# Performance work log

Hardware: AMD Instinct MI355X
Metric: run time of the kernel (lower is better)

Reference implementation:

```python
import jax, jax.numpy as jnp
import numpy as np

B, S, T, D = 64, 50, 200, 128
IN2, H = 128, 64
NEG = -1e10


def setup_inputs() -> dict:
    key = jax.random.key(0)
    k1, k2, k3, k4, k5, k6, k7, k8 = jax.random.split(key, 8)
    inp = jax.random.normal(k1, (B, S, T, D), dtype=jnp.float32)
    z = jax.random.normal(k2, (B, S, IN2), dtype=jnp.float32)
    mask = jax.random.randint(k3, (B, S, T), 0, 2, dtype=jnp.int32)
    # torch nn.Linear weights: [out, in]
    W1 = jax.random.normal(k4, (H, D), dtype=jnp.float32) / np.sqrt(D)
    W2_w = jax.random.normal(k5, (H, IN2), dtype=jnp.float32) / np.sqrt(IN2)
    W2_b = jax.random.normal(k6, (H,), dtype=jnp.float32) * 0.01
    V_w = jax.random.normal(k7, (1, H), dtype=jnp.float32) / np.sqrt(H)
    V_b = jax.random.normal(k8, (1,), dtype=jnp.float32) * 0.01
    return {"input": inp, "z": z, "mask": mask, "W1": W1,
            "W2_w": W2_w, "W2_b": W2_b, "V_w": V_w, "V_b": V_b}


def reference(input, z, mask, W1, W2_w, W2_b, V_w, V_b):
    # w1h: [B,S,T,H]
    w1h = jnp.einsum('bstd,hd->bsth', input, W1)
    # w2h: [B,S,H] (Linear with bias), broadcast over T
    w2h = jnp.einsum('bsd,hd->bsh', z, W2_w) + W2_b
    u = jnp.tanh(w1h + w2h[:, :, None, :])           # [B,S,T,H]
    att = jnp.einsum('bsth,h->bst', u, V_w[0]) + V_b[0]  # [B,S,T]
    att = jnp.where(mask == 0, NEG, att)
    att = jax.nn.softmax(att, axis=2)
    out = jnp.einsum('bst,bstd->bsd', att, input)    # [B,S,D]
    return out
```

## Files before the change

kernel.cpp:

```cpp
#include <hip/hip_runtime.h>

#define Tdim 200
#define Ddim 128
#define Hdim 64
#define NBS  3200
#define NEGV (-1e10f)

typedef _Float16 f16x8 __attribute__((ext_vector_type(8)));
typedef float    floatx4 __attribute__((ext_vector_type(4)));

__device__ __forceinline__ unsigned int packf16(float a, float b) {
    _Float16 ha = (_Float16)a, hb = (_Float16)b;
    unsigned int ua = *(unsigned short*)&ha, ub = *(unsigned short*)&hb;
    return ua | (ub << 16);
}

__device__ __forceinline__ float ftanh(float x) {
    float e = __expf(2.0f * x);
    return 1.0f - 2.0f * __builtin_amdgcn_rcpf(e + 1.0f);
}

__global__ __launch_bounds__(256, 3) void attn_main(
    const float* __restrict__ X, const float* __restrict__ z,
    const int* __restrict__ mask,
    const float* __restrict__ W1, const float* __restrict__ W2w,
    const float* __restrict__ W2b,
    const float* __restrict__ Vw, const float* __restrict__ Vb,
    float* __restrict__ out)
{
    __shared__ __align__(16) unsigned short xs[Tdim * 128];
    __shared__ float attL[Tdim];
    __shared__ float red[8];
    __shared__ float w2hL[Hdim];

    const int tid = threadIdx.x;
    const int bs  = blockIdx.x;
    const float* __restrict__ Xb = X + (size_t)bs * (Tdim * Ddim);
    const int lane = tid & 63;
    const int wv   = tid >> 6;
    const int l15  = lane & 15, quad = lane >> 4;

    int mval = 1;
    if (tid < Tdim) mval = mask[bs * Tdim + tid];

    {
        const int h = tid >> 2, q = tid & 3;
        const float4* zp = (const float4*)(z + (size_t)bs * 128 + q * 32);
        const float4* wp = (const float4*)(W2w + h * 128 + q * 32);
        float a = 0.f;
        #pragma unroll
        for (int i = 0; i < 8; ++i) {
            float4 zv = zp[i], wv4 = wp[i];
            a = fmaf(zv.x, wv4.x, a); a = fmaf(zv.y, wv4.y, a);
            a = fmaf(zv.z, wv4.z, a); a = fmaf(zv.w, wv4.w, a);
        }
        a += __shfl_xor(a, 1);
        a += __shfl_xor(a, 2);
        if (q == 0) w2hL[h] = a + W2b[h];
    }
    __syncthreads();

    const int R0  = wv * 48;
    const int nIt = (wv == 3) ? 28 : 24;
    #pragma unroll 4
    for (int i = 0; i < nIt; ++i) {
        int j = i * 64 + lane;
        int t = R0 + (j >> 5), dq = j & 31;
        float4 v = *(const float4*)(Xb + t * Ddim + dq * 4);
        unsigned int lo = packf16(v.x, v.y);
        unsigned int hi = packf16(v.z, v.w);
        int u16 = t * 16 + ((dq >> 1) ^ (t & 15));
        *(uint2*)((char*)xs + u16 * 16 + (dq & 1) * 8) = make_uint2(lo, hi);
    }

    f16x8 bfrag[4][4];
    #pragma unroll
    for (int n = 0; n < 4; ++n)
        #pragma unroll
        for (int ks = 0; ks < 4; ++ks) {
            const float* wp = W1 + (n * 16 + l15) * 128 + ks * 32 + quad * 8;
            float4 v0 = *(const float4*)wp;
            float4 v1 = *(const float4*)(wp + 4);
            uint4 u = make_uint4(packf16(v0.x, v0.y), packf16(v0.z, v0.w),
                                 packf16(v1.x, v1.y), packf16(v1.z, v1.w));
            bfrag[n][ks] = *(f16x8*)&u;
        }

    const float Vb0 = Vb[0];
    float vwr[4], w2[4];
    #pragma unroll
    for (int n = 0; n < 4; ++n) {
        vwr[n] = Vw[l15 + 16 * n];
        w2[n]  = w2hL[l15 + 16 * n];
    }

    const int mtEnd = (wv == 3) ? 13 : wv * 3 + 3;
    for (int mt = wv * 3; mt < mtEnd; ++mt) {
        const int t0 = (mt == 12) ? 184 : mt * 16;
        const int trow = t0 + l15;
        floatx4 acc[4];
        #pragma unroll
        for (int n = 0; n < 4; ++n) acc[n] = (floatx4){0.f, 0.f, 0.f, 0.f};
        f16x8 afrag[4];
        #pragma unroll
        for (int ks = 0; ks < 4; ++ks) {
            int u16 = trow * 16 + (((ks << 2) + quad) ^ (trow & 15));
            afrag[ks] = *(const f16x8*)(xs + u16 * 8);
        }
        #pragma unroll
        for (int n = 0; n < 4; ++n)
            #pragma unroll
            for (int ks = 0; ks < 4; ++ks)
                acc[n] = __builtin_amdgcn_mfma_f32_16x16x32_f16(afrag[ks], bfrag[n][ks], acc[n], 0, 0, 0);

        float s0 = 0.f, s1 = 0.f, s2 = 0.f, s3 = 0.f;
        #pragma unroll
        for (int n = 0; n < 4; ++n) {
            s0 = fmaf(ftanh(acc[n][0] + w2[n]), vwr[n], s0);
            s1 = fmaf(ftanh(acc[n][1] + w2[n]), vwr[n], s1);
            s2 = fmaf(ftanh(acc[n][2] + w2[n]), vwr[n], s2);
            s3 = fmaf(ftanh(acc[n][3] + w2[n]), vwr[n], s3);
        }
        #pragma unroll
        for (int m = 1; m < 16; m <<= 1) {
            s0 += __shfl_xor(s0, m);
            s1 += __shfl_xor(s1, m);
            s2 += __shfl_xor(s2, m);
            s3 += __shfl_xor(s3, m);
        }
        if (l15 == 0) {
            const int tb = t0 + quad * 4;
            attL[tb]     = s0 + Vb0;
            attL[tb + 1] = s1 + Vb0;
            attL[tb + 2] = s2 + Vb0;
            attL[tb + 3] = s3 + Vb0;
        }
    }
    __syncthreads();

    float l = -3e38f;
    if (tid < Tdim) {
        l = attL[tid];
        if (mval == 0) l = NEGV;
    }
    float m = l;
    #pragma unroll
    for (int off = 32; off > 0; off >>= 1) m = fmaxf(m, __shfl_xor(m, off));
    if (lane == 0) red[wv] = m;
    __syncthreads();
    const float M = fmaxf(fmaxf(red[0], red[1]), fmaxf(red[2], red[3]));
    float p = __expf(l - M);
    float sm = p;
    #pragma unroll
    for (int off = 32; off > 0; off >>= 1) sm += __shfl_xor(sm, off);
    if (lane == 0) red[4 + wv] = sm;
    __syncthreads();
    const float S = (red[4] + red[5]) + (red[6] + red[7]);
    if (tid < Tdim) attL[tid] = p / S;
    __syncthreads();

    {
        const int dblk = 4 * wv + (lane & 3);
        const int tg   = lane >> 2;
        float o0=0.f,o1=0.f,o2=0.f,o3=0.f,o4=0.f,o5=0.f,o6=0.f,o7=0.f;
        #pragma unroll 4
        for (int t = tg; t < Tdim; t += 16) {
            int u16 = t * 16 + (dblk ^ (t & 15));
            f16x8 xv = *(const f16x8*)(xs + u16 * 8);
            float a = attL[t];
            o0 = fmaf((float)xv[0], a, o0);
            o1 = fmaf((float)xv[1], a, o1);
            o2 = fmaf((float)xv[2], a, o2);
            o3 = fmaf((float)xv[3], a, o3);
            o4 = fmaf((float)xv[4], a, o4);
            o5 = fmaf((float)xv[5], a, o5);
            o6 = fmaf((float)xv[6], a, o6);
            o7 = fmaf((float)xv[7], a, o7);
        }
        #pragma unroll
        for (int m2 = 4; m2 <= 32; m2 <<= 1) {
            o0 += __shfl_xor(o0, m2); o1 += __shfl_xor(o1, m2);
            o2 += __shfl_xor(o2, m2); o3 += __shfl_xor(o3, m2);
            o4 += __shfl_xor(o4, m2); o5 += __shfl_xor(o5, m2);
            o6 += __shfl_xor(o6, m2); o7 += __shfl_xor(o7, m2);
        }
        if (tg == 0) {
            float* op = out + bs * Ddim + dblk * 8;
            *(float4*)op       = make_float4(o0, o1, o2, o3);
            *(float4*)(op + 4) = make_float4(o4, o5, o6, o7);
        }
    }
}

extern "C" void kernel_launch(void* const* d_in, const int* in_sizes, int n_in,
                              void* d_out, int out_size, void* d_ws, size_t ws_size,
                              hipStream_t stream) {
    const float* X    = (const float*)d_in[0];
    const float* z    = (const float*)d_in[1];
    const int*   mask = (const int*)d_in[2];
    const float* W1   = (const float*)d_in[3];
    const float* W2w  = (const float*)d_in[4];
    const float* W2b  = (const float*)d_in[5];
    const float* Vw   = (const float*)d_in[6];
    const float* Vb   = (const float*)d_in[7];
    float* out = (float*)d_out;

    attn_main<<<NBS, 256, 0, stream>>>(X, z, mask, W1, W2w, W2b, Vw, Vb, out);
}
```

Measured before the change: 473.7 us.

## Compute W2h per-lane in registers and fuse softmax into weighted sum

Removes the shared-memory W2h stage and its block barrier by having each lane compute its four W2h values directly from z and W2w, then reduce them with cross-lane shuffles. The mask is applied when attention logits are written, and the softmax max and sum are computed redundantly within each wave over all T values. This drops three barriers and the reduction scratch array. The cost is more redundant global loads of W2w/z per lane and more exp work per wave; masked-out t beyond T get probability zero via a -3e38 sentinel, and the read from xs is clamped to row 0 so it stays in bounds.

```diff
diff --git a/kernel.cpp b/kernel.cpp
--- a/kernel.cpp
+++ b/kernel.cpp
@@ -30,35 +30,19 @@
 {
     __shared__ __align__(16) unsigned short xs[Tdim * 128];
     __shared__ float attL[Tdim];
-    __shared__ float red[8];
-    __shared__ float w2hL[Hdim];
 
     const int tid = threadIdx.x;
     const int bs  = blockIdx.x;
     const float* __restrict__ Xb = X + (size_t)bs * (Tdim * Ddim);
+    const int* __restrict__ maskb = mask + bs * Tdim;
     const int lane = tid & 63;
     const int wv   = tid >> 6;
     const int l15  = lane & 15, quad = lane >> 4;
 
-    int mval = 1;
-    if (tid < Tdim) mval = mask[bs * Tdim + tid];
-
-    {
-        const int h = tid >> 2, q = tid & 3;
-        const float4* zp = (const float4*)(z + (size_t)bs * 128 + q * 32);
-        const float4* wp = (const float4*)(W2w + h * 128 + q * 32);
-        float a = 0.f;
-        #pragma unroll
-        for (int i = 0; i < 8; ++i) {
-            float4 zv = zp[i], wv4 = wp[i];
-            a = fmaf(zv.x, wv4.x, a); a = fmaf(zv.y, wv4.y, a);
-            a = fmaf(zv.z, wv4.z, a); a = fmaf(zv.w, wv4.w, a);
-        }
-        a += __shfl_xor(a, 1);
-        a += __shfl_xor(a, 2);
-        if (q == 0) w2hL[h] = a + W2b[h];
-    }
-    __syncthreads();
+    if (tid < Tdim) {
+        int mv_ = maskb[tid];
+        asm volatile("" :: "v"(mv_));
+    }
 
     const int R0  = wv * 48;
     const int nIt = (wv == 3) ? 28 : 24;
@@ -73,6 +57,32 @@
         *(uint2*)((char*)xs + u16 * 16 + (dq & 1) * 8) = make_uint2(lo, hi);
     }
 
+    float w2[4];
+    {
+        const float4* zp = (const float4*)(z + (size_t)bs * 128 + quad * 32);
+        float4 zv[8];
+        #pragma unroll
+        for (int i = 0; i < 8; ++i) zv[i] = zp[i];
+        #pragma unroll
+        for (int n = 0; n < 4; ++n) {
+            const float4* wp = (const float4*)(W2w + (l15 + 16 * n) * 128 + quad * 32);
+            float a = 0.f;
+            #pragma unroll
+            for (int i = 0; i < 8; ++i) {
+                float4 wv4 = wp[i];
+                a = fmaf(zv[i].x, wv4.x, a); a = fmaf(zv[i].y, wv4.y, a);
+                a = fmaf(zv[i].z, wv4.z, a); a = fmaf(zv[i].w, wv4.w, a);
+            }
+            w2[n] = a;
+        }
+        #pragma unroll
+        for (int n = 0; n < 4; ++n) {
+            w2[n] += __shfl_xor(w2[n], 16);
+            w2[n] += __shfl_xor(w2[n], 32);
+            w2[n] += W2b[l15 + 16 * n];
+        }
+    }
+
     f16x8 bfrag[4][4];
     #pragma unroll
     for (int n = 0; n < 4; ++n)
@@ -87,12 +97,9 @@
         }
 
     const float Vb0 = Vb[0];
-    float vwr[4], w2[4];
+    float vwr[4];
     #pragma unroll
-    for (int n = 0; n < 4; ++n) {
-        vwr[n] = Vw[l15 + 16 * n];
-        w2[n]  = w2hL[l15 + 16 * n];
-    }
+    for (int n = 0; n < 4; ++n) vwr[n] = Vw[l15 + 16 * n];
 
     const int mtEnd = (wv == 3) ? 13 : wv * 3 + 3;
     for (int mt = wv * 3; mt < mtEnd; ++mt) {
@@ -130,44 +137,47 @@
         }
         if (l15 == 0) {
             const int tb = t0 + quad * 4;
-            attL[tb]     = s0 + Vb0;
-            attL[tb + 1] = s1 + Vb0;
-            attL[tb + 2] = s2 + Vb0;
-            attL[tb + 3] = s3 + Vb0;
+            const int4 mv = *(const int4*)(maskb + tb);
+            attL[tb]     = (mv.x == 0) ? NEGV : s0 + Vb0;
+            attL[tb + 1] = (mv.y == 0) ? NEGV : s1 + Vb0;
+            attL[tb + 2] = (mv.z == 0) ? NEGV : s2 + Vb0;
+            attL[tb + 3] = (mv.w == 0) ? NEGV : s3 + Vb0;
         }
     }
     __syncthreads();
 
-    float l = -3e38f;
-    if (tid < Tdim) {
-        l = attL[tid];
-        if (mval == 0) l = NEGV;
-    }
-    float m = l;
-    #pragma unroll
-    for (int off = 32; off > 0; off >>= 1) m = fmaxf(m, __shfl_xor(m, off));
-    if (lane == 0) red[wv] = m;
-    __syncthreads();
-    const float M = fmaxf(fmaxf(red[0], red[1]), fmaxf(red[2], red[3]));
-    float p = __expf(l - M);
-    float sm = p;
-    #pragma unroll
-    for (int off = 32; off > 0; off >>= 1) sm += __shfl_xor(sm, off);
-    if (lane == 0) red[4 + wv] = sm;
-    __syncthreads();
-    const float S = (red[4] + red[5]) + (red[6] + red[7]);
-    if (tid < Tdim) attL[tid] = p / S;
-    __syncthreads();
-
     {
-        const int dblk = 4 * wv + (lane & 3);
-        const int tg   = lane >> 2;
+        const int tg = lane >> 2, dblk = 4 * wv + (lane & 3);
+        float pv[13];
+        float mx = -3e38f;
+        #pragma unroll
+        for (int k = 0; k < 13; ++k) {
+            int t = tg + 16 * k;
+            float lk = (t < Tdim) ? attL[t] : -3e38f;
+            pv[k] = lk;
+            mx = fmaxf(mx, lk);
+        }
+        #pragma unroll
+        for (int off = 4; off <= 32; off <<= 1) mx = fmaxf(mx, __shfl_xor(mx, off));
+        float sum = 0.f;
+        #pragma unroll
+        for (int k = 0; k < 13; ++k) {
+            float p = __expf(pv[k] - mx);
+            pv[k] = p;
+            sum += p;
+        }
+        #pragma unroll
+        for (int off = 4; off <= 32; off <<= 1) sum += __shfl_xor(sum, off);
+        const float inv = 1.0f / sum;
+
         float o0=0.f,o1=0.f,o2=0.f,o3=0.f,o4=0.f,o5=0.f,o6=0.f,o7=0.f;
-        #pragma unroll 4
-        for (int t = tg; t < Tdim; t += 16) {
-            int u16 = t * 16 + (dblk ^ (t & 15));
+        #pragma unroll
+        for (int k = 0; k < 13; ++k) {
+            int t = tg + 16 * k;
+            int tcl = (t < Tdim) ? t : 0;
+            float a = pv[k] * inv;
+            int u16 = tcl * 16 + (dblk ^ (tcl & 15));
             f16x8 xv = *(const f16x8*)(xs + u16 * 8);
-            float a = attL[t];
             o0 = fmaf((float)xv[0], a, o0);
             o1 = fmaf((float)xv[1], a, o1);
             o2 = fmaf((float)xv[2], a, o2);
```

Measured after the change: 499.3 us. +5.4%, slower.
